# Kernel optimization log

Measured on AMD Instinct MI355X. Metric: run time of the kernel, lower is better.

Reference implementation:

```python
import jax, jax.numpy as jnp
import numpy as np

B, S, E, H = 32, 2048, 512, 512


def setup_inputs() -> dict:
    key = jax.random.key(0)
    ks = jax.random.split(key, 6)
    scale = 1.0 / np.sqrt(H)  # PyTorch LSTM init range
    x = jax.random.normal(ks[0], (B, S, E), dtype=jnp.float32)
    lengths = jax.random.randint(ks[1], (B,), 1, S + 1, dtype=jnp.int32)
    W_ih = jax.random.uniform(ks[2], (4 * H, E), jnp.float32, -scale, scale)
    W_hh = jax.random.uniform(ks[3], (4 * H, H), jnp.float32, -scale, scale)
    b_ih = jax.random.uniform(ks[4], (4 * H,), jnp.float32, -scale, scale)
    b_hh = jax.random.uniform(ks[5], (4 * H,), jnp.float32, -scale, scale)
    return {"x": x, "lengths": lengths, "W_ih": W_ih, "W_hh": W_hh,
            "b_ih": b_ih, "b_hh": b_hh}


def _lstm_scan(x, W_ih, W_hh, b_ih, b_hh):
    # x: [B, S, E]. Precompute input projections for all timesteps (one big GEMM).
    x_proj = jnp.einsum('bse,ge->bsg', x, W_ih) + (b_ih + b_hh)  # [B, S, 4H]
    x_proj_t = jnp.swapaxes(x_proj, 0, 1)  # [S, B, 4H]

    def step(carry, xp_t):
        h, c = carry
        gates = xp_t + h @ W_hh.T  # [B, 4H]
        i, f, g, o = jnp.split(gates, 4, axis=-1)  # PyTorch gate order i,f,g,o
        i = jax.nn.sigmoid(i)
        f = jax.nn.sigmoid(f)
        g = jnp.tanh(g)
        o = jax.nn.sigmoid(o)
        c = f * c + i * g
        h = o * jnp.tanh(c)
        return (h, c), h

    h0 = jnp.zeros((B, H), dtype=x.dtype)
    c0 = jnp.zeros((B, H), dtype=x.dtype)
    (_, _), hs = jax.lax.scan(step, (h0, c0), x_proj_t)  # hs: [S, B, H]
    return hs


def reference(x, lengths, W_ih, W_hh, b_ih, b_hh):
    hs = _lstm_scan(x, W_ih, W_hh, b_ih, b_hh)  # [S, B, H]
    # zero-mask outputs at positions >= length (matches __maskLSTMOutput)
    mask = (jnp.arange(S)[:, None] < lengths[None, :]).astype(hs.dtype)  # [S, B]
    out = (hs * mask[:, :, None]).transpose(1, 0, 2)[:, :, None, :]  # [B, S, 1, H]
    # hidden state captured at t = length-1 per sequence (matches __updateHiddenOutput)
    hidden = hs[lengths - 1, jnp.arange(B)][None, :, :]  # [1, B, H]
    return (out, lengths, hidden)
```

## Files before the change

### kernel.cpp

```cpp
#include <hip/hip_runtime.h>


typedef __attribute__((ext_vector_type(8))) __bf16 bf16x8;
typedef __attribute__((ext_vector_type(8))) short short8;
typedef __attribute__((ext_vector_type(4))) float floatx4;
typedef __attribute__((ext_vector_type(2))) unsigned uint32x2;

#define XP_OFF   0ull
#define XP_BYTES (2048ull * 32ull * 2048ull * 2ull)
#define HPK_OFF  (XP_OFF + XP_BYTES)
#define HPK_BYTES (2ull * 16384ull * 4ull)
#define BIAS_OFF (HPK_OFF + HPK_BYTES)
#define FLAG_OFF (BIAS_OFF + 8192ull)
#define WS_NEED  (FLAG_OFF + 256ull)

#define LEN_OFF_F    33554432
#define HIDDEN_OFF_F 33554464

__device__ inline float sigm(float x) { return 1.f / (1.f + __expf(-x)); }
__device__ inline float tanh_(float x) {
  float e = __expf(-2.f * fabsf(x));
  float r = (1.f - e) / (1.f + e);
  return x >= 0.f ? r : -r;
}

__device__ inline void cvt_hilo8(const float* v, bf16x8& hi, bf16x8& lo) {
#pragma unroll
  for (int i = 0; i < 8; ++i) {
    __bf16 h = (__bf16)v[i];
    hi[i] = h;
    lo[i] = (__bf16)(v[i] - (float)h);
  }
}

__device__ inline float bf16f(unsigned short u) {
  union { unsigned u; float f; } c; c.u = ((unsigned)u) << 16; return c.f;
}

__global__ __launch_bounds__(256) void prep_kernel(
    const float* __restrict__ bih, const float* __restrict__ bhh,
    const int* __restrict__ len, float* __restrict__ biasp,
    unsigned* __restrict__ hpk, unsigned* __restrict__ flags,
    float* __restrict__ outf) {
  const int tid = threadIdx.x;
  for (int i = tid; i < 2048; i += 256) {
    int rowg = (i & 3) * 512 + (i >> 4) * 4 + ((i >> 2) & 3);
    biasp[i] = bih[rowg] + bhh[rowg];
  }
  for (int i = tid; i < 32768; i += 256) hpk[i] = 0u;
  if (tid < 64) flags[tid] = 0u;
  if (tid < 32) outf[LEN_OFF_F + tid] = (float)len[tid];
}

__global__ __launch_bounds__(256) void xproj_gemm(
    const float* __restrict__ x, const float* __restrict__ Wih,
    const float* __restrict__ biasp, __bf16* __restrict__ xp) {
  __shared__ short Ash[64 * 40], Asl[64 * 40], Bsh[64 * 40], Bsl[64 * 40];
  const int tid = threadIdx.x;
  const int w = tid >> 6, lane = tid & 63, ln = lane & 15, kq = lane >> 4;
  const int ntile = blockIdx.x & 31, mtile = blockIdx.x >> 5;
  const int srow = tid >> 2, sseg = tid & 3;

  const size_t a_base = (size_t)(mtile * 64 + srow) * 512 + sseg * 8;
  const int np_s = ntile * 64 + srow;
  const int rowg = (np_s & 3) * 512 + (np_s >> 4) * 4 + ((np_s >> 2) & 3);
  const size_t b_base = (size_t)rowg * 512 + sseg * 8;

  floatx4 acc[4] = {{0,0,0,0},{0,0,0,0},{0,0,0,0},{0,0,0,0}};

  for (int k0 = 0; k0 < 512; k0 += 32) {
    floatx4 a0 = *(const floatx4*)(x + a_base + k0);
    floatx4 a1 = *(const floatx4*)(x + a_base + k0 + 4);
    floatx4 b0 = *(const floatx4*)(Wih + b_base + k0);
    floatx4 b1 = *(const floatx4*)(Wih + b_base + k0 + 4);
    __syncthreads();
    {
      float va[8] = {a0[0],a0[1],a0[2],a0[3],a1[0],a1[1],a1[2],a1[3]};
      bf16x8 hi, lo; cvt_hilo8(va, hi, lo);
      *(short8*)&Ash[srow * 40 + sseg * 8] = __builtin_bit_cast(short8, hi);
      *(short8*)&Asl[srow * 40 + sseg * 8] = __builtin_bit_cast(short8, lo);
      float vb[8] = {b0[0],b0[1],b0[2],b0[3],b1[0],b1[1],b1[2],b1[3]};
      cvt_hilo8(vb, hi, lo);
      *(short8*)&Bsh[srow * 40 + sseg * 8] = __builtin_bit_cast(short8, hi);
      *(short8*)&Bsl[srow * 40 + sseg * 8] = __builtin_bit_cast(short8, lo);
    }
    __syncthreads();
    bf16x8 ah = __builtin_bit_cast(bf16x8, *(const short8*)&Ash[(16 * w + ln) * 40 + kq * 8]);
    bf16x8 al = __builtin_bit_cast(bf16x8, *(const short8*)&Asl[(16 * w + ln) * 40 + kq * 8]);
#pragma unroll
    for (int nt = 0; nt < 4; ++nt) {
      bf16x8 bh = __builtin_bit_cast(bf16x8, *(const short8*)&Bsh[(nt * 16 + ln) * 40 + kq * 8]);
      bf16x8 bl = __builtin_bit_cast(bf16x8, *(const short8*)&Bsl[(nt * 16 + ln) * 40 + kq * 8]);
      acc[nt] = __builtin_amdgcn_mfma_f32_16x16x32_bf16(ah, bh, acc[nt], 0, 0, 0);
      acc[nt] = __builtin_amdgcn_mfma_f32_16x16x32_bf16(al, bh, acc[nt], 0, 0, 0);
      acc[nt] = __builtin_amdgcn_mfma_f32_16x16x32_bf16(ah, bl, acc[nt], 0, 0, 0);
    }
  }
#pragma unroll
  for (int nt = 0; nt < 4; ++nt) {
    const int npg = ntile * 64 + nt * 16 + ln;
    const float bs = biasp[npg];
#pragma unroll
    for (int r = 0; r < 4; ++r) {
      const int m = mtile * 64 + w * 16 + kq * 4 + r;
      const int s = m & 2047, b = m >> 11;
      xp[(size_t)(s * 32 + b) * 2048 + npg] = (__bf16)(acc[nt][r] + bs);
    }
  }
}

__global__ __launch_bounds__(256, 1) void lstm_rec(
    const float* __restrict__ Whh, const int* __restrict__ lengths,
    const __bf16* __restrict__ xp, float* __restrict__ out,
    float* __restrict__ hid, unsigned* __restrict__ hpk,
    unsigned* __restrict__ flags) {
  __shared__ short Hh[16 * 512];
  __shared__ short Hl[16 * 512];
  __shared__ float Part[4 * 1088];

  const int tid = threadIdx.x;
  const int w = tid >> 6, lane = tid & 63, ln = lane & 15, kq = lane >> 4;
  const int bh = blockIdx.x >> 5;
  const int ug = blockIdx.x & 31;
  const int b0 = bh * 16;

  bf16x8 whi[4][4], wlo[4][4];
#pragma unroll
  for (int nt = 0; nt < 4; ++nt) {
    const int rowg = (ln & 3) * 512 + (ug * 4 + nt) * 4 + (ln >> 2);
#pragma unroll
    for (int kc = 0; kc < 4; ++kc) {
      const int k = w * 128 + kc * 32 + kq * 8;
      floatx4 f0 = *(const floatx4*)(Whh + (size_t)rowg * 512 + k);
      floatx4 f1 = *(const floatx4*)(Whh + (size_t)rowg * 512 + k + 4);
      float v[8] = {f0[0],f0[1],f0[2],f0[3],f1[0],f1[1],f1[2],f1[3]};
      cvt_hilo8(v, whi[nt][kc], wlo[nt][kc]);
    }
  }

  const int m_e = tid >> 4, ue = tid & 15;
  const int b_e = b0 + m_e, u_e = ug * 16 + ue;
  const int lenb = lengths[b_e];
  float cst = 0.f, hcap = 0.f;

  const __bf16* xpb = xp + (size_t)b_e * 2048 + ug * 64 + (ue >> 2) * 16 + (ue & 3) * 4;
  uint32x2 xpcur = *(const uint32x2*)xpb;
  uint32x2 xpnext;

  unsigned* myflag = flags + bh * 32 + ug;
  const unsigned* pollp = flags + bh * 32 + (lane & 31);

  for (int t = 0; t < 2048; ++t) {
    if (w == 0 && t > 0) {
      for (;;) {
        unsigned f = __hip_atomic_load(pollp, __ATOMIC_RELAXED,
                                       __HIP_MEMORY_SCOPE_AGENT);
        if (__ballot(f < (unsigned)t) == 0ull) break;
        __builtin_amdgcn_s_sleep(1);
      }
    }
    __syncthreads();
    const unsigned* src = hpk + (t & 1) * 16384 + b0 * 512;
    unsigned long long v[16];
#pragma unroll
    for (int k = 0; k < 16; ++k)
      v[k] = __hip_atomic_load(
          (const unsigned long long*)(src + k * 512 + tid * 2),
          __ATOMIC_RELAXED, __HIP_MEMORY_SCOPE_AGENT);
    {
      const int tn = (t + 1 < 2048) ? t + 1 : 2047;
      xpnext = *(const uint32x2*)(xpb + (size_t)tn * 65536);
    }
    {
      const int g = tid >> 2;
#pragma unroll
      for (int k = 0; k < 16; ++k) {
        const unsigned w0 = (unsigned)v[k], w1 = (unsigned)(v[k] >> 32);
        const int d = k * 512 + ((g ^ (k & 7)) * 8) + (tid & 3) * 2;
        *(unsigned*)&Hh[d] = (w0 >> 16) | (w1 & 0xffff0000u);
        *(unsigned*)&Hl[d] = (w0 & 0xffffu) | (w1 << 16);
      }
    }
    __syncthreads();
    floatx4 acc[4] = {{0,0,0,0},{0,0,0,0},{0,0,0,0},{0,0,0,0}};
#pragma unroll
    for (int kc = 0; kc < 4; ++kc) {
      const int g = w * 16 + kc * 4 + kq;
      const int d = ln * 512 + ((g ^ (ln & 7)) * 8);
      bf16x8 ah = __builtin_bit_cast(bf16x8, *(const short8*)&Hh[d]);
      bf16x8 al = __builtin_bit_cast(bf16x8, *(const short8*)&Hl[d]);
#pragma unroll
      for (int nt = 0; nt < 4; ++nt) {
        acc[nt] = __builtin_amdgcn_mfma_f32_16x16x32_bf16(ah, whi[nt][kc], acc[nt], 0, 0, 0);
        acc[nt] = __builtin_amdgcn_mfma_f32_16x16x32_bf16(al, whi[nt][kc], acc[nt], 0, 0, 0);
        acc[nt] = __builtin_amdgcn_mfma_f32_16x16x32_bf16(ah, wlo[nt][kc], acc[nt], 0, 0, 0);
      }
    }
#pragma unroll
    for (int nt = 0; nt < 4; ++nt)
#pragma unroll
      for (int r4 = 0; r4 < 4; ++r4)
        Part[w * 1088 + nt * 272 + (kq * 4 + r4) * 16 + ln] = acc[nt][r4];
    __syncthreads();
    {
      const int pb = (ue >> 2) * 272 + m_e * 16 + (ue & 3) * 4;
      floatx4 p0 = *(const floatx4*)&Part[pb];
      floatx4 p1 = *(const floatx4*)&Part[1088 + pb];
      floatx4 p2 = *(const floatx4*)&Part[2176 + pb];
      floatx4 p3 = *(const floatx4*)&Part[3264 + pb];
      const float xg0 = bf16f((unsigned short)(xpcur[0] & 0xffffu));
      const float xg1 = bf16f((unsigned short)(xpcur[0] >> 16));
      const float xg2 = bf16f((unsigned short)(xpcur[1] & 0xffffu));
      const float xg3 = bf16f((unsigned short)(xpcur[1] >> 16));
      const float pi = xg0 + p0[0] + p1[0] + p2[0] + p3[0];
      const float pf = xg1 + p0[1] + p1[1] + p2[1] + p3[1];
      const float pg = xg2 + p0[2] + p1[2] + p2[2] + p3[2];
      const float po = xg3 + p0[3] + p1[3] + p2[3] + p3[3];
      const float gi_ = sigm(pi), gf = sigm(pf), gg = tanh_(pg), go = sigm(po);
      cst = gf * cst + gi_ * gg;
      const float hv = go * tanh_(cst);
      const __bf16 hb = (__bf16)hv;
      const __bf16 lb = (__bf16)(hv - (float)hb);
      const unsigned pk =
          ((unsigned)__builtin_bit_cast(unsigned short, hb) << 16) |
          (unsigned)__builtin_bit_cast(unsigned short, lb);
      __hip_atomic_store(hpk + ((t + 1) & 1) * 16384 + b_e * 512 + u_e, pk,
                         __ATOMIC_RELAXED, __HIP_MEMORY_SCOPE_AGENT);
      asm volatile("s_waitcnt vmcnt(0)" ::: "memory");
      __syncthreads();
      if (tid == 0)
        __hip_atomic_store(myflag, (unsigned)(t + 1), __ATOMIC_RELAXED,
                           __HIP_MEMORY_SCOPE_AGENT);
      out[((size_t)b_e * 2048 + t) * 512 + u_e] = (t < lenb) ? hv : 0.f;
      if (t == lenb - 1) hcap = hv;
    }
    xpcur = xpnext;
  }
  hid[b_e * 512 + u_e] = hcap;
}

extern "C" void kernel_launch(void* const* d_in, const int* in_sizes, int n_in,
                              void* d_out, int out_size, void* d_ws, size_t ws_size,
                              hipStream_t stream) {
  const float* x = (const float*)d_in[0];
  const int* lengths = (const int*)d_in[1];
  const float* Wih = (const float*)d_in[2];
  const float* Whh = (const float*)d_in[3];
  const float* bih = (const float*)d_in[4];
  const float* bhh = (const float*)d_in[5];
  float* outf = (float*)d_out;
  char* ws = (char*)d_ws;
  if (ws_size < WS_NEED) return;

  float* biasp = (float*)(ws + BIAS_OFF);
  __bf16* xp = (__bf16*)(ws + XP_OFF);
  unsigned* hpk = (unsigned*)(ws + HPK_OFF);
  unsigned* flags = (unsigned*)(ws + FLAG_OFF);

  prep_kernel<<<1, 256, 0, stream>>>(bih, bhh, lengths, biasp, hpk, flags, outf);
  xproj_gemm<<<32768, 256, 0, stream>>>(x, Wih, biasp, xp);
  lstm_rec<<<64, 256, 0, stream>>>(Whh, lengths, xp, outf,
                                   outf + HIDDEN_OFF_F, hpk, flags);
}
```

Before: 7.750 ms.

## Replace per-block flag barrier with step-tagged hidden-state words polled directly

Each published hidden value becomes a 64-bit word holding the step index next to the packed bf16 hi/lo value. Consumers poll the data itself until every tag matches the current step, so the separate flag write, the store drain, and the block-wide barrier before it are gone. This takes a store-wait-flag-poll round trip off the serial recurrence's critical path. In exchange each block reads twice as many bytes per step, and the W_hh K-ordering is permuted to match the new interleaved layout.

```diff
diff --git a/kernel.cpp b/kernel.cpp
--- a/kernel.cpp
+++ b/kernel.cpp
@@ -9,10 +9,9 @@
 #define XP_OFF   0ull
 #define XP_BYTES (2048ull * 32ull * 2048ull * 2ull)
 #define HPK_OFF  (XP_OFF + XP_BYTES)
-#define HPK_BYTES (2ull * 16384ull * 4ull)
+#define HPK_BYTES (2ull * 16384ull * 8ull)
 #define BIAS_OFF (HPK_OFF + HPK_BYTES)
-#define FLAG_OFF (BIAS_OFF + 8192ull)
-#define WS_NEED  (FLAG_OFF + 256ull)
+#define WS_NEED  (BIAS_OFF + 8192ull)
 
 #define LEN_OFF_F    33554432
 #define HIDDEN_OFF_F 33554464
@@ -40,15 +39,13 @@
 __global__ __launch_bounds__(256) void prep_kernel(
     const float* __restrict__ bih, const float* __restrict__ bhh,
     const int* __restrict__ len, float* __restrict__ biasp,
-    unsigned* __restrict__ hpk, unsigned* __restrict__ flags,
-    float* __restrict__ outf) {
+    unsigned long long* __restrict__ hpk, float* __restrict__ outf) {
   const int tid = threadIdx.x;
   for (int i = tid; i < 2048; i += 256) {
     int rowg = (i & 3) * 512 + (i >> 4) * 4 + ((i >> 2) & 3);
     biasp[i] = bih[rowg] + bhh[rowg];
   }
-  for (int i = tid; i < 32768; i += 256) hpk[i] = 0u;
-  if (tid < 64) flags[tid] = 0u;
+  for (int i = tid; i < 32768; i += 256) hpk[i] = 0ull;
   if (tid < 32) outf[LEN_OFF_F + tid] = (float)len[tid];
 }
 
@@ -112,8 +109,7 @@
 __global__ __launch_bounds__(256, 1) void lstm_rec(
     const float* __restrict__ Whh, const int* __restrict__ lengths,
     const __bf16* __restrict__ xp, float* __restrict__ out,
-    float* __restrict__ hid, unsigned* __restrict__ hpk,
-    unsigned* __restrict__ flags) {
+    float* __restrict__ hid, unsigned long long* __restrict__ hpk) {
   __shared__ short Hh[16 * 512];
   __shared__ short Hl[16 * 512];
   __shared__ float Part[4 * 1088];
@@ -130,10 +126,10 @@
     const int rowg = (ln & 3) * 512 + (ug * 4 + nt) * 4 + (ln >> 2);
 #pragma unroll
     for (int kc = 0; kc < 4; ++kc) {
-      const int k = w * 128 + kc * 32 + kq * 8;
-      floatx4 f0 = *(const floatx4*)(Whh + (size_t)rowg * 512 + k);
-      floatx4 f1 = *(const floatx4*)(Whh + (size_t)rowg * 512 + k + 4);
-      float v[8] = {f0[0],f0[1],f0[2],f0[3],f1[0],f1[1],f1[2],f1[3]};
+      const int h0 = w * 64 + kc * 16 + kq * 4;
+      floatx4 f0 = *(const floatx4*)(Whh + (size_t)rowg * 512 + h0);
+      floatx4 f1 = *(const floatx4*)(Whh + (size_t)rowg * 512 + h0 + 256);
+      float v[8] = {f0[0],f1[0],f0[1],f1[1],f0[2],f1[2],f0[3],f1[3]};
       cvt_hilo8(v, whi[nt][kc], wlo[nt][kc]);
     }
   }
@@ -147,38 +143,42 @@
   uint32x2 xpcur = *(const uint32x2*)xpb;
   uint32x2 xpnext;
 
-  unsigned* myflag = flags + bh * 32 + ug;
-  const unsigned* pollp = flags + bh * 32 + (lane & 31);
+  unsigned long long* pub = hpk + b_e * 512 + u_e;
+  const unsigned long long* pollb = hpk + b0 * 512 + tid;
 
   for (int t = 0; t < 2048; ++t) {
-    if (w == 0 && t > 0) {
-      for (;;) {
-        unsigned f = __hip_atomic_load(pollp, __ATOMIC_RELAXED,
-                                       __HIP_MEMORY_SCOPE_AGENT);
-        if (__ballot(f < (unsigned)t) == 0ull) break;
-        __builtin_amdgcn_s_sleep(1);
-      }
-    }
-    __syncthreads();
-    const unsigned* src = hpk + (t & 1) * 16384 + b0 * 512;
-    unsigned long long v[16];
-#pragma unroll
-    for (int k = 0; k < 16; ++k)
-      v[k] = __hip_atomic_load(
-          (const unsigned long long*)(src + k * 512 + tid * 2),
-          __ATOMIC_RELAXED, __HIP_MEMORY_SCOPE_AGENT);
     {
       const int tn = (t + 1 < 2048) ? t + 1 : 2047;
       xpnext = *(const uint32x2*)(xpb + (size_t)tn * 65536);
     }
+    const unsigned long long* src = pollb + (t & 1) * 16384;
+    unsigned long long e[32];
+    bool ok = false;
+    for (;;) {
+      if (!ok) {
+#pragma unroll
+        for (int k = 0; k < 16; ++k) {
+          e[2 * k] = __hip_atomic_load(src + k * 512, __ATOMIC_RELAXED,
+                                       __HIP_MEMORY_SCOPE_AGENT);
+          e[2 * k + 1] = __hip_atomic_load(src + k * 512 + 256, __ATOMIC_RELAXED,
+                                           __HIP_MEMORY_SCOPE_AGENT);
+        }
+        ok = true;
+#pragma unroll
+        for (int k = 0; k < 32; ++k)
+          ok &= ((unsigned)(e[k] >> 32) == (unsigned)t);
+      }
+      if (__ballot(!ok) == 0ull) break;
+      __builtin_amdgcn_s_sleep(1);
+    }
     {
       const int g = tid >> 2;
 #pragma unroll
       for (int k = 0; k < 16; ++k) {
-        const unsigned w0 = (unsigned)v[k], w1 = (unsigned)(v[k] >> 32);
+        const unsigned d0 = (unsigned)e[2 * k], d1 = (unsigned)e[2 * k + 1];
         const int d = k * 512 + ((g ^ (k & 7)) * 8) + (tid & 3) * 2;
-        *(unsigned*)&Hh[d] = (w0 >> 16) | (w1 & 0xffff0000u);
-        *(unsigned*)&Hl[d] = (w0 & 0xffffu) | (w1 << 16);
+        *(unsigned*)&Hh[d] = (d0 >> 16) | (d1 & 0xffff0000u);
+        *(unsigned*)&Hl[d] = (d0 & 0xffffu) | (d1 << 16);
       }
     }
     __syncthreads();
@@ -224,13 +224,10 @@
       const unsigned pk =
           ((unsigned)__builtin_bit_cast(unsigned short, hb) << 16) |
           (unsigned)__builtin_bit_cast(unsigned short, lb);
-      __hip_atomic_store(hpk + ((t + 1) & 1) * 16384 + b_e * 512 + u_e, pk,
+      __hip_atomic_store(pub + ((t + 1) & 1) * 16384,
+                         ((unsigned long long)(unsigned)(t + 1) << 32) |
+                             (unsigned long long)pk,
                          __ATOMIC_RELAXED, __HIP_MEMORY_SCOPE_AGENT);
-      asm volatile("s_waitcnt vmcnt(0)" ::: "memory");
-      __syncthreads();
-      if (tid == 0)
-        __hip_atomic_store(myflag, (unsigned)(t + 1), __ATOMIC_RELAXED,
-                           __HIP_MEMORY_SCOPE_AGENT);
       out[((size_t)b_e * 2048 + t) * 512 + u_e] = (t < lenb) ? hv : 0.f;
       if (t == lenb - 1) hcap = hv;
     }
@@ -254,11 +251,10 @@
 
   float* biasp = (float*)(ws + BIAS_OFF);
   __bf16* xp = (__bf16*)(ws + XP_OFF);
-  unsigned* hpk = (unsigned*)(ws + HPK_OFF);
-  unsigned* flags = (unsigned*)(ws + FLAG_OFF);
-
-  prep_kernel<<<1, 256, 0, stream>>>(bih, bhh, lengths, biasp, hpk, flags, outf);
+  unsigned long long* hpk = (unsigned long long*)(ws + HPK_OFF);
+
+  prep_kernel<<<1, 256, 0, stream>>>(bih, bhh, lengths, biasp, hpk, outf);
   xproj_gemm<<<32768, 256, 0, stream>>>(x, Wih, biasp, xp);
   lstm_rec<<<64, 256, 0, stream>>>(Whh, lengths, xp, outf,
-                                   outf + HIDDEN_OFF_F, hpk, flags);
-}
+                                   outf + HIDDEN_OFF_F, hpk);
+}
```

Result: slower. 8.097 ms (+4.5%).
